# Kernel optimization log

Hardware: AMD Instinct MI355X
Metric: run time of the kernel (lower is better)

## Reference

```python
import jax, jax.numpy as jnp
import numpy as np

B, N, L, H, D = 1, 2048, 256, 24, 128
DX, DY = H * D, 1536          # dim_x = 3072, dim_y = 1536
LV = 200                      # valid text tokens
TOTAL = N + LV                # packed token count
EPS = 1e-6


def rms_norm(t):
    return t * jax.lax.rsqrt(jnp.mean(jnp.square(t), axis=-1, keepdims=True) + EPS)


def setup_inputs() -> dict:
    key = jax.random.key(0)
    ks = jax.random.split(key, 16)
    s = 0.02
    theta = jax.random.uniform(ks[4], (N, H, D // 2), jnp.float32, 0.0, 2.0 * np.pi)
    return {
        "x": jax.random.normal(ks[0], (B, N, DX), jnp.float32),
        "y": jax.random.normal(ks[1], (B, L, DY), jnp.float32),
        "scale_x": jax.random.normal(ks[2], (B, DX), jnp.float32) * 0.1,
        "scale_y": jax.random.normal(ks[3], (B, DY), jnp.float32) * 0.1,
        "rope_cos": jnp.cos(theta),
        "rope_sin": jnp.sin(theta),
        "W_qkv_x": jax.random.normal(ks[5], (3 * DX, DX), jnp.float32) * s,
        "b_qkv_x": jax.random.normal(ks[6], (3 * DX,), jnp.float32) * s,
        "W_qkv_y": jax.random.normal(ks[7], (3 * DX, DY), jnp.float32) * s,
        "b_qkv_y": jax.random.normal(ks[8], (3 * DX,), jnp.float32) * s,
        "q_norm_x": jnp.ones((D,), jnp.float32),
        "k_norm_x": jnp.ones((D,), jnp.float32),
        "q_norm_y": jnp.ones((D,), jnp.float32),
        "k_norm_y": jnp.ones((D,), jnp.float32),
        "W_proj_x": jax.random.normal(ks[9], (DX, DX), jnp.float32) * s,
        "b_proj_x": jax.random.normal(ks[10], (DX,), jnp.float32) * s,
        "W_proj_y": jax.random.normal(ks[11], (DY, DX), jnp.float32) * s,
        "b_proj_y": jax.random.normal(ks[12], (DY,), jnp.float32) * s,
        "valid_token_indices": jnp.arange(TOTAL, dtype=jnp.int64)
        if jax.config.jax_enable_x64 else jnp.arange(TOTAL, dtype=jnp.int32),
    }


def _rope(t, cos, sin):
    # t: (B, N, H, D); cos/sin: (N, H, D/2); real interleaved RoPE
    te, to = t[..., 0::2], t[..., 1::2]
    return jnp.stack([te * cos - to * sin, te * sin + to * cos], axis=-1).reshape(t.shape)


def reference(x, y, scale_x, scale_y, rope_cos, rope_sin,
              W_qkv_x, b_qkv_x, W_qkv_y, b_qkv_y,
              q_norm_x, k_norm_x, q_norm_y, k_norm_y,
              W_proj_x, b_proj_x, W_proj_y, b_proj_y,
              valid_token_indices):
    # modulated RMSNorm + fused qkv projections
    xm = rms_norm(x) * (1.0 + scale_x[:, None, :])                 # (B,N,DX)
    qkv_x = (xm @ W_qkv_x.T + b_qkv_x).reshape(B, N, 3, H, D)
    q_x, k_x, v_x = qkv_x[:, :, 0], qkv_x[:, :, 1], qkv_x[:, :, 2]

    ym = rms_norm(y) * (1.0 + scale_y[:, None, :])                 # (B,L,DY)
    qkv_y = (ym @ W_qkv_y.T + b_qkv_y).reshape(B, L, 3, H, D)
    q_y, k_y, v_y = qkv_y[:, :, 0], qkv_y[:, :, 1], qkv_y[:, :, 2]

    # QK-norm (per-head RMSNorm with learnable weight) + RoPE on visual stream
    q_x = _rope(rms_norm(q_x) * q_norm_x, rope_cos, rope_sin)
    k_x = _rope(rms_norm(k_x) * k_norm_x, rope_cos, rope_sin)
    q_y = rms_norm(q_y) * q_norm_y
    k_y = rms_norm(k_y) * k_norm_y

    # unify_streams: concat streams, gather valid tokens -> packed (TOTAL,H,D)
    q = jnp.concatenate([q_x, q_y], axis=1).reshape(B * (N + L), H, D)[valid_token_indices]
    k = jnp.concatenate([k_x, k_y], axis=1).reshape(B * (N + L), H, D)[valid_token_indices]
    v = jnp.concatenate([v_x, v_y], axis=1).reshape(B * (N + L), H, D)[valid_token_indices]

    # flash varlen attention, B=1 -> single full non-causal segment
    scale = 1.0 / np.sqrt(D)
    scores = jnp.einsum("qhd,khd->hqk", q, k) * scale              # (H,T,T)
    attn = jax.nn.softmax(scores, axis=-1)
    out = jnp.einsum("hqk,khd->qhd", attn, v).reshape(TOTAL, H * D)

    # pad_and_split_xy: scatter packed outputs back to (B, N+L, DX)
    full = jnp.zeros((B * (N + L), H * D), out.dtype).at[valid_token_indices].set(out)
    full = full.reshape(B, N + L, H * D)
    x_out = full[:, :N] @ W_proj_x.T + b_proj_x                    # (B,N,DX)
    y_out = full[:, N:] @ W_proj_y.T + b_proj_y                    # (B,L,DY)
    return x_out, y_out
```

## Files before the change

### kernel.cpp

```cpp
#include <hip/hip_runtime.h>
#include <math.h>

#define NX 2048
#define LY 256
#define NH 24
#define DH 128
#define DXC 3072
#define DYC 1536
#define NLTOK 2304
#define NTOT 2248
#define RMS_EPS 1e-6f

typedef __bf16 bf16x8 __attribute__((ext_vector_type(8)));
typedef float f32x4 __attribute__((ext_vector_type(4)));

static __device__ __forceinline__ unsigned short f2bf(float f) {
    union { float f; unsigned int u; } x; x.f = f;
    unsigned int r = (x.u + 0x7fffu + ((x.u >> 16) & 1u)) >> 16;
    return (unsigned short)r;
}
static __device__ __forceinline__ float bf2f(unsigned short u) {
    union { unsigned int u; float f; } x; x.u = ((unsigned int)u) << 16;
    return x.f;
}
static __device__ __forceinline__ unsigned int pack2(float lo, float hi) {
    return (unsigned int)f2bf(lo) | ((unsigned int)f2bf(hi) << 16);
}
static __device__ __forceinline__ void split4(float4 f, uint2& h, uint2& l) {
    unsigned int ux = __float_as_uint(f.x), uy = __float_as_uint(f.y);
    unsigned int uz = __float_as_uint(f.z), uw = __float_as_uint(f.w);
    h.x = (ux >> 16) | (uy & 0xffff0000u);
    h.y = (uz >> 16) | (uw & 0xffff0000u);
    float lx = f.x - __uint_as_float(ux & 0xffff0000u);
    float ly = f.y - __uint_as_float(uy & 0xffff0000u);
    float lz = f.z - __uint_as_float(uz & 0xffff0000u);
    float lw = f.w - __uint_as_float(uw & 0xffff0000u);
    l.x = pack2(lx, ly);
    l.y = pack2(lz, lw);
}

__global__ __launch_bounds__(256) void rmsnorm_scale_split_kernel(
    const float* __restrict__ in, const float* __restrict__ scale,
    unsigned short* __restrict__ out_hi, unsigned short* __restrict__ out_lo,
    int cols)
{
    const int row = blockIdx.x;
    const int tid = threadIdx.x;
    const float* rp = in + (size_t)row * cols;
    const int nv = cols >> 2;
    float4 vals[3];
    float ss = 0.f;
    int cnt = 0;
    for (int c4 = tid; c4 < nv; c4 += 256) {
        float4 v = ((const float4*)rp)[c4];
        vals[cnt++] = v;
        ss += v.x * v.x + v.y * v.y + v.z * v.z + v.w * v.w;
    }
#pragma unroll
    for (int m = 1; m < 64; m <<= 1) ss += __shfl_xor(ss, m, 64);
    __shared__ float red[4];
    if ((tid & 63) == 0) red[tid >> 6] = ss;
    __syncthreads();
    const float tot = red[0] + red[1] + red[2] + red[3];
    const float r = rsqrtf(tot / (float)cols + RMS_EPS);
    unsigned short* oh = out_hi + (size_t)row * cols;
    unsigned short* ol = out_lo + (size_t)row * cols;
    cnt = 0;
    for (int c4 = tid; c4 < nv; c4 += 256) {
        float4 v = vals[cnt++];
        float4 s = ((const float4*)scale)[c4];
        float4 o;
        o.x = v.x * r * (1.f + s.x);
        o.y = v.y * r * (1.f + s.y);
        o.z = v.z * r * (1.f + s.z);
        o.w = v.w * r * (1.f + s.w);
        uint2 h, l;
        split4(o, h, l);
        ((uint2*)oh)[c4] = h;
        ((uint2*)ol)[c4] = l;
    }
}

__global__ __launch_bounds__(256) void gemm_split_kernel(
    const unsigned short* __restrict__ Ahg, const unsigned short* __restrict__ Alg,
    const float* __restrict__ Bg, const float* __restrict__ bias,
    float* __restrict__ C,
    unsigned short* __restrict__ qp, unsigned short* __restrict__ kp,
    unsigned short* __restrict__ vp,
    int Nc, int K, int mode, int row_off)
{
    __shared__ unsigned short Ah[128 * 40];
    __shared__ unsigned short Al[128 * 40];
    __shared__ unsigned short Bh[128 * 40];
    __shared__ unsigned short Bl[128 * 40];

    const int tid = threadIdx.x;
    const int n0 = blockIdx.x * 128;
    const int m0 = blockIdx.y * 128;
    const int wave = tid >> 6, lane = tid & 63;
    const int quad = lane >> 4, ln = lane & 15;
    const int wm = wave >> 1, wn = wave & 1;
    const int sr = tid >> 1;
    const int sk = (tid & 1) * 16;

    const unsigned short* Abh = Ahg + (size_t)(m0 + sr) * K + sk;
    const unsigned short* Abl = Alg + (size_t)(m0 + sr) * K + sk;
    const float* Bb = Bg + (size_t)(n0 + sr) * K + sk;

    f32x4 acc[4][4];
#pragma unroll
    for (int i = 0; i < 4; ++i)
#pragma unroll
        for (int j = 0; j < 4; ++j) acc[i][j] = (f32x4){0.f, 0.f, 0.f, 0.f};

    uint4 pah0 = *(const uint4*)Abh;
    uint4 pah1 = *(const uint4*)(Abh + 8);
    uint4 pal0 = *(const uint4*)Abl;
    uint4 pal1 = *(const uint4*)(Abl + 8);
    uint4 pbh0, pbh1, pbl0, pbl1;
    {
        float4 b0 = ((const float4*)Bb)[0];
        float4 b1 = ((const float4*)Bb)[1];
        float4 b2 = ((const float4*)Bb)[2];
        float4 b3 = ((const float4*)Bb)[3];
        uint2 h0, l0, h1, l1, h2, l2, h3, l3;
        split4(b0, h0, l0); split4(b1, h1, l1);
        split4(b2, h2, l2); split4(b3, h3, l3);
        pbh0 = make_uint4(h0.x, h0.y, h1.x, h1.y);
        pbh1 = make_uint4(h2.x, h2.y, h3.x, h3.y);
        pbl0 = make_uint4(l0.x, l0.y, l1.x, l1.y);
        pbl1 = make_uint4(l2.x, l2.y, l3.x, l3.y);
    }

    for (int k0 = 0; k0 < K; k0 += 32) {
        __syncthreads();
        *(uint4*)&Ah[sr * 40 + sk]     = pah0;
        *(uint4*)&Ah[sr * 40 + sk + 8] = pah1;
        *(uint4*)&Al[sr * 40 + sk]     = pal0;
        *(uint4*)&Al[sr * 40 + sk + 8] = pal1;
        *(uint4*)&Bh[sr * 40 + sk]     = pbh0;
        *(uint4*)&Bh[sr * 40 + sk + 8] = pbh1;
        *(uint4*)&Bl[sr * 40 + sk]     = pbl0;
        *(uint4*)&Bl[sr * 40 + sk + 8] = pbl1;
        __syncthreads();

        if (k0 + 32 < K) {
            const unsigned short* ah2 = Abh + k0 + 32;
            const unsigned short* al2 = Abl + k0 + 32;
            const float* b2p = Bb + k0 + 32;
            pah0 = *(const uint4*)ah2;  pah1 = *(const uint4*)(ah2 + 8);
            pal0 = *(const uint4*)al2;  pal1 = *(const uint4*)(al2 + 8);
            float4 b0 = ((const float4*)b2p)[0];
            float4 b1 = ((const float4*)b2p)[1];
            float4 b2 = ((const float4*)b2p)[2];
            float4 b3 = ((const float4*)b2p)[3];
            uint2 h0, l0, h1, l1, h2, l2, h3, l3;
            split4(b0, h0, l0); split4(b1, h1, l1);
            split4(b2, h2, l2); split4(b3, h3, l3);
            pbh0 = make_uint4(h0.x, h0.y, h1.x, h1.y);
            pbh1 = make_uint4(h2.x, h2.y, h3.x, h3.y);
            pbl0 = make_uint4(l0.x, l0.y, l1.x, l1.y);
            pbl1 = make_uint4(l2.x, l2.y, l3.x, l3.y);
        }

        bf16x8 afh[4], afl[4];
#pragma unroll
        for (int mt = 0; mt < 4; ++mt) {
            const int rr = (wm * 64 + mt * 16 + ln) * 40 + quad * 8;
            afh[mt] = __builtin_bit_cast(bf16x8, *(const uint4*)&Ah[rr]);
            afl[mt] = __builtin_bit_cast(bf16x8, *(const uint4*)&Al[rr]);
        }
#pragma unroll
        for (int nt = 0; nt < 4; ++nt) {
            const int rr = (wn * 64 + nt * 16 + ln) * 40 + quad * 8;
            bf16x8 bfh = __builtin_bit_cast(bf16x8, *(const uint4*)&Bh[rr]);
            bf16x8 bfl = __builtin_bit_cast(bf16x8, *(const uint4*)&Bl[rr]);
#pragma unroll
            for (int mt = 0; mt < 4; ++mt) {
                acc[mt][nt] = __builtin_amdgcn_mfma_f32_16x16x32_bf16(afh[mt], bfh, acc[mt][nt], 0, 0, 0);
                acc[mt][nt] = __builtin_amdgcn_mfma_f32_16x16x32_bf16(afl[mt], bfh, acc[mt][nt], 0, 0, 0);
                acc[mt][nt] = __builtin_amdgcn_mfma_f32_16x16x32_bf16(afh[mt], bfl, acc[mt][nt], 0, 0, 0);
            }
        }
    }

    float bias4[4];
#pragma unroll
    for (int nt = 0; nt < 4; ++nt) bias4[nt] = bias[n0 + wn * 64 + nt * 16 + ln];

    if (mode == 0) {
#pragma unroll
        for (int mt = 0; mt < 4; ++mt) {
            const int rbase = m0 + wm * 64 + mt * 16 + quad * 4;
#pragma unroll
            for (int reg = 0; reg < 4; ++reg) {
                float* cp = C + (size_t)(rbase + reg) * Nc + n0 + wn * 64 + ln;
#pragma unroll
                for (int nt = 0; nt < 4; ++nt)
                    cp[nt * 16] = acc[mt][nt][reg] + bias4[nt];
            }
        }
    } else {
        const int part = n0 / DXC;
        unsigned short* dst = (part == 0) ? qp : (part == 1) ? kp : vp;
        const int cc = (n0 % DXC) + wn * 64 + ln;
#pragma unroll
        for (int mt = 0; mt < 4; ++mt) {
            const int rbase = row_off + m0 + wm * 64 + mt * 16 + quad * 4;
#pragma unroll
            for (int reg = 0; reg < 4; ++reg) {
                unsigned short* cp = dst + (size_t)(rbase + reg) * DXC + cc;
#pragma unroll
                for (int nt = 0; nt < 4; ++nt)
                    cp[nt * 16] = f2bf(acc[mt][nt][reg] + bias4[nt]);
            }
        }
    }
}

__global__ __launch_bounds__(128) void qknorm_rope_kernel(
    unsigned short* __restrict__ qb, unsigned short* __restrict__ kb,
    const float* __restrict__ qnx, const float* __restrict__ knx,
    const float* __restrict__ qny, const float* __restrict__ kny,
    const float* __restrict__ cosp, const float* __restrict__ sinp)
{
    const int bx = blockIdx.x;
    const int which = bx & 1;
    const int h = (bx >> 1) % NH;
    const int t = bx / (2 * NH);
    unsigned short* p = (which ? kb : qb) + (size_t)t * DXC + h * DH;
    const int d = threadIdx.x;
    const float v = bf2f(p[d]);
    float ss = v * v;
#pragma unroll
    for (int m = 1; m < 64; m <<= 1) ss += __shfl_xor(ss, m, 64);
    __shared__ float red[2];
    if ((d & 63) == 0) red[d >> 6] = ss;
    __syncthreads();
    const float tot = red[0] + red[1];
    const float r = rsqrtf(tot * (1.f / 128.f) + RMS_EPS);
    const float* w = (t < NX) ? (which ? knx : qnx) : (which ? kny : qny);
    const float nv = v * r * w[d];
    float outv = nv;
    if (t < NX) {
        const int pidx = d >> 1;
        const float cs = cosp[((size_t)t * NH + h) * 64 + pidx];
        const float sn = sinp[((size_t)t * NH + h) * 64 + pidx];
        const float partner = __shfl_xor(nv, 1, 64);
        outv = ((d & 1) == 0) ? (nv * cs - partner * sn)
                              : (partner * sn + nv * cs);
    }
    p[d] = f2bf(outv);
}

#define BQ 64
#define BKV 64
#define NQT ((NTOT + BQ - 1) / BQ)
#define ATTN_SCALE 0.08838834764831845f

__global__ __launch_bounds__(256, 3) void attn_kernel(
    const unsigned short* __restrict__ qb, const unsigned short* __restrict__ kb,
    const unsigned short* __restrict__ vb,
    unsigned short* __restrict__ out_hi, unsigned short* __restrict__ out_lo,
    const int* __restrict__ idx)
{
    __shared__ unsigned short Ks[64 * 136];
    __shared__ unsigned int   Vt[128 * 36];
    __shared__ unsigned short Ps[4][16 * 72];

    const int h  = blockIdx.x / NQT;
    const int qt = blockIdx.x % NQT;
    const int q0 = qt * BQ;
    const int tid  = threadIdx.x;
    const int wave = tid >> 6;
    const int lane = tid & 63;
    const int quad = lane >> 4;
    const int ln   = lane & 15;
    const int ch   = tid & 15;
    const int rb   = tid >> 4;

    bf16x8 aq[4];
    {
        const int qi = q0 + wave * 16 + ln;
        if (qi < NTOT) {
            const unsigned short* qrow = qb + (size_t)idx[qi] * DXC + h * DH;
#pragma unroll
            for (int c = 0; c < 4; ++c)
                aq[c] = __builtin_bit_cast(bf16x8, *(const uint4*)(qrow + c * 32 + quad * 8));
        } else {
            const uint4 z = make_uint4(0, 0, 0, 0);
#pragma unroll
            for (int c = 0; c < 4; ++c) aq[c] = __builtin_bit_cast(bf16x8, z);
        }
    }

    f32x4 o[8];
#pragma unroll
    for (int dt = 0; dt < 8; ++dt) o[dt] = (f32x4){0.f, 0.f, 0.f, 0.f};
    float m_i[4] = {-1e30f, -1e30f, -1e30f, -1e30f};
    float l_i[4] = {0.f, 0.f, 0.f, 0.f};

    uint4 kreg[4], vra[2], vrb[2];
    const uint4 z4 = make_uint4(0, 0, 0, 0);
    auto prefetchKV = [&](int kv0) {
#pragma unroll
        for (int it = 0; it < 4; ++it) {
            const int ki = kv0 + rb + it * 16;
            kreg[it] = (ki < NTOT)
                ? *(const uint4*)(kb + (size_t)idx[ki] * DXC + h * DH + ch * 8) : z4;
        }
#pragma unroll
        for (int it = 0; it < 2; ++it) {
            const int pr = rb + it * 16;
            const int k0i = kv0 + pr * 2, k1i = k0i + 1;
            vra[it] = (k0i < NTOT)
                ? *(const uint4*)(vb + (size_t)idx[k0i] * DXC + h * DH + ch * 8) : z4;
            vrb[it] = (k1i < NTOT)
                ? *(const uint4*)(vb + (size_t)idx[k1i] * DXC + h * DH + ch * 8) : z4;
        }
    };
    prefetchKV(0);

    for (int kv0 = 0; kv0 < NTOT; kv0 += BKV) {
        __syncthreads();
#pragma unroll
        for (int it = 0; it < 4; ++it)
            *(uint4*)&Ks[(rb + it * 16) * 136 + ch * 8] = kreg[it];
#pragma unroll
        for (int it = 0; it < 2; ++it) {
            const int pr = rb + it * 16;
            const uint4 a = vra[it], b = vrb[it];
            unsigned int w[8];
            w[0] = (a.x & 0xffffu) | (b.x << 16);  w[1] = (a.x >> 16) | (b.x & 0xffff0000u);
            w[2] = (a.y & 0xffffu) | (b.y << 16);  w[3] = (a.y >> 16) | (b.y & 0xffff0000u);
            w[4] = (a.z & 0xffffu) | (b.z << 16);  w[5] = (a.z >> 16) | (b.z & 0xffff0000u);
            w[6] = (a.w & 0xffffu) | (b.w << 16);  w[7] = (a.w >> 16) | (b.w & 0xffff0000u);
#pragma unroll
            for (int s = 0; s < 8; ++s) {
                const int e = (s + ch) & 7;
                Vt[(ch * 8 + e) * 36 + pr] = w[e];
            }
        }
        __syncthreads();

        if (kv0 + BKV < NTOT) prefetchKV(kv0 + BKV);

        f32x4 sc[4];
        __builtin_amdgcn_s_setprio(1);
#pragma unroll
        for (int t = 0; t < 4; ++t) {
            sc[t] = (f32x4){0.f, 0.f, 0.f, 0.f};
#pragma unroll
            for (int c = 0; c < 4; ++c) {
                bf16x8 bk = __builtin_bit_cast(bf16x8,
                    *(const uint4*)&Ks[(t * 16 + ln) * 136 + c * 32 + quad * 8]);
                sc[t] = __builtin_amdgcn_mfma_f32_16x16x32_bf16(aq[c], bk, sc[t], 0, 0, 0);
            }
        }
        __builtin_amdgcn_s_setprio(0);

        float alpha[4];
#pragma unroll
        for (int r = 0; r < 4; ++r) {
            float mt = -1e30f;
#pragma unroll
            for (int t = 0; t < 4; ++t) {
                float sv = sc[t][r] * ATTN_SCALE;
                if (kv0 + t * 16 + ln >= NTOT) sv = -1e30f;
                sc[t][r] = sv;
                mt = fmaxf(mt, sv);
            }
#pragma unroll
            for (int mm = 1; mm < 16; mm <<= 1) mt = fmaxf(mt, __shfl_xor(mt, mm, 64));
            const float mn = fmaxf(m_i[r], mt);
            alpha[r] = __expf(m_i[r] - mn);
            m_i[r] = mn;
            float rs = 0.f;
#pragma unroll
            for (int t = 0; t < 4; ++t) {
                const float pv = __expf(sc[t][r] - mn);
                sc[t][r] = pv;
                rs += pv;
            }
#pragma unroll
            for (int mm = 1; mm < 16; mm <<= 1) rs += __shfl_xor(rs, mm, 64);
            l_i[r] = l_i[r] * alpha[r] + rs;
        }

        unsigned short* psw = Ps[wave];
#pragma unroll
        for (int t = 0; t < 4; ++t)
#pragma unroll
            for (int r = 0; r < 4; ++r)
                psw[(quad * 4 + r) * 72 + t * 16 + ln] = f2bf(sc[t][r]);

#pragma unroll
        for (int dt = 0; dt < 8; ++dt)
#pragma unroll
            for (int r = 0; r < 4; ++r) o[dt][r] *= alpha[r];

        bf16x8 ap0 = __builtin_bit_cast(bf16x8, *(const uint4*)&psw[ln * 72 + quad * 8]);
        bf16x8 ap1 = __builtin_bit_cast(bf16x8, *(const uint4*)&psw[ln * 72 + 32 + quad * 8]);
        __builtin_amdgcn_s_setprio(1);
#pragma unroll
        for (int dt = 0; dt < 8; ++dt) {
            bf16x8 bv0 = __builtin_bit_cast(bf16x8,
                *(const uint4*)&Vt[(dt * 16 + ln) * 36 + quad * 4]);
            o[dt] = __builtin_amdgcn_mfma_f32_16x16x32_bf16(ap0, bv0, o[dt], 0, 0, 0);
            bf16x8 bv1 = __builtin_bit_cast(bf16x8,
                *(const uint4*)&Vt[(dt * 16 + ln) * 36 + 16 + quad * 4]);
            o[dt] = __builtin_amdgcn_mfma_f32_16x16x32_bf16(ap1, bv1, o[dt], 0, 0, 0);
        }
        __builtin_amdgcn_s_setprio(0);
    }

#pragma unroll
    for (int r = 0; r < 4; ++r) {
        const int qrow = q0 + wave * 16 + quad * 4 + r;
        if (qrow >= NTOT) continue;
        const int tok = idx[qrow];
        const float inv = 1.f / l_i[r];
        unsigned short* hp = out_hi + (size_t)tok * DXC + h * DH + ln;
        unsigned short* lp = out_lo + (size_t)tok * DXC + h * DH + ln;
#pragma unroll
        for (int dt = 0; dt < 8; ++dt) {
            const float v = o[dt][r] * inv;
            const unsigned int u = __float_as_uint(v);
            hp[dt * 16] = (unsigned short)(u >> 16);
            lp[dt * 16] = f2bf(v - __uint_as_float(u & 0xffff0000u));
        }
    }
}

extern "C" void kernel_launch(void* const* d_in, const int* in_sizes, int n_in,
                              void* d_out, int out_size, void* d_ws, size_t ws_size,
                              hipStream_t stream)
{
    const float* x        = (const float*)d_in[0];
    const float* y        = (const float*)d_in[1];
    const float* scale_x  = (const float*)d_in[2];
    const float* scale_y  = (const float*)d_in[3];
    const float* rope_cos = (const float*)d_in[4];
    const float* rope_sin = (const float*)d_in[5];
    const float* W_qkv_x  = (const float*)d_in[6];
    const float* b_qkv_x  = (const float*)d_in[7];
    const float* W_qkv_y  = (const float*)d_in[8];
    const float* b_qkv_y  = (const float*)d_in[9];
    const float* q_norm_x = (const float*)d_in[10];
    const float* k_norm_x = (const float*)d_in[11];
    const float* q_norm_y = (const float*)d_in[12];
    const float* k_norm_y = (const float*)d_in[13];
    const float* W_proj_x = (const float*)d_in[14];
    const float* b_proj_x = (const float*)d_in[15];
    const float* W_proj_y = (const float*)d_in[16];
    const float* b_proj_y = (const float*)d_in[17];
    const int*   vidx     = (const int*)d_in[18];
    float* out = (float*)d_out;

    unsigned short* wsu = (unsigned short*)d_ws;
    const size_t SEG = (size_t)NLTOK * DXC;
    unsigned short* q16     = wsu;
    unsigned short* k16     = wsu + SEG;
    unsigned short* v16     = wsu + 2 * SEG;
    unsigned short* attn_hi = wsu + 3 * SEG;
    unsigned short* attn_lo = wsu + 4 * SEG;
    unsigned short* xm_hi   = wsu + 5 * SEG;
    unsigned short* xm_lo   = wsu + 6 * SEG;
    unsigned short* ym_hi   = xm_hi + (size_t)NX * DXC;
    unsigned short* ym_lo   = xm_lo + (size_t)NX * DXC;

    hipMemsetAsync(attn_hi, 0, 2 * SEG * sizeof(unsigned short), stream);

    rmsnorm_scale_split_kernel<<<NX, 256, 0, stream>>>(x, scale_x, xm_hi, xm_lo, DXC);
    rmsnorm_scale_split_kernel<<<LY, 256, 0, stream>>>(y, scale_y, ym_hi, ym_lo, DYC);

    gemm_split_kernel<<<dim3(9216 / 128, NX / 128), 256, 0, stream>>>(
        xm_hi, xm_lo, W_qkv_x, b_qkv_x, nullptr, q16, k16, v16, 0, DXC, 1, 0);
    gemm_split_kernel<<<dim3(9216 / 128, LY / 128), 256, 0, stream>>>(
        ym_hi, ym_lo, W_qkv_y, b_qkv_y, nullptr, q16, k16, v16, 0, DYC, 1, NX);

    qknorm_rope_kernel<<<NLTOK * NH * 2, 128, 0, stream>>>(
        q16, k16, q_norm_x, k_norm_x, q_norm_y, k_norm_y, rope_cos, rope_sin);

    attn_kernel<<<NH * NQT, 256, 0, stream>>>(q16, k16, v16, attn_hi, attn_lo, vidx);

    gemm_split_kernel<<<dim3(DXC / 128, NX / 128), 256, 0, stream>>>(
        attn_hi, attn_lo, W_proj_x, b_proj_x, out, nullptr, nullptr, nullptr,
        DXC, DXC, 0, 0);
    gemm_split_kernel<<<dim3(DYC / 128, LY / 128), 256, 0, stream>>>(
        attn_hi + (size_t)NX * DXC, attn_lo + (size_t)NX * DXC,
        W_proj_y, b_proj_y, out + (size_t)NX * DXC, nullptr, nullptr, nullptr,
        DYC, DXC, 0, 0);
}
```

Measured before the change: 1.560 ms.

## Split attention KV range across two blocks and merge partials in combine kernel

Attention blocks now each process half of the key/value sequence, doubling the grid to improve CU utilization and reduce tail imbalance. Each split writes unnormalized partial outputs plus running max and sum to a workspace, and a new combine kernel merges them with log-sum-exp weights and scatters to token positions. This adds extra global traffic for the partials, an extra kernel launch, and a memset into reused workspace.

```diff
diff --git a/kernel.cpp b/kernel.cpp
--- a/kernel.cpp
+++ b/kernel.cpp
@@ -9,6 +9,8 @@
 #define DYC 1536
 #define NLTOK 2304
 #define NTOT 2248
+#define KVSPLIT 1124
+#define OPS 130
 #define RMS_EPS 1e-6f
 
 typedef __bf16 bf16x8 __attribute__((ext_vector_type(8)));
@@ -261,7 +263,7 @@
 __global__ __launch_bounds__(256, 3) void attn_kernel(
     const unsigned short* __restrict__ qb, const unsigned short* __restrict__ kb,
     const unsigned short* __restrict__ vb,
-    unsigned short* __restrict__ out_hi, unsigned short* __restrict__ out_lo,
+    unsigned short* __restrict__ ophi, unsigned short* __restrict__ oplo,
     const int* __restrict__ idx)
 {
     __shared__ unsigned short Ks[64 * 136];
@@ -270,6 +272,9 @@
 
     const int h  = blockIdx.x / NQT;
     const int qt = blockIdx.x % NQT;
+    const int s  = blockIdx.y;
+    const int kv_beg = s * KVSPLIT;
+    const int kv_end = (s == 0) ? KVSPLIT : NTOT;
     const int q0 = qt * BQ;
     const int tid  = threadIdx.x;
     const int wave = tid >> 6;
@@ -306,22 +311,22 @@
 #pragma unroll
         for (int it = 0; it < 4; ++it) {
             const int ki = kv0 + rb + it * 16;
-            kreg[it] = (ki < NTOT)
+            kreg[it] = (ki < kv_end)
                 ? *(const uint4*)(kb + (size_t)idx[ki] * DXC + h * DH + ch * 8) : z4;
         }
 #pragma unroll
         for (int it = 0; it < 2; ++it) {
             const int pr = rb + it * 16;
             const int k0i = kv0 + pr * 2, k1i = k0i + 1;
-            vra[it] = (k0i < NTOT)
+            vra[it] = (k0i < kv_end)
                 ? *(const uint4*)(vb + (size_t)idx[k0i] * DXC + h * DH + ch * 8) : z4;
-            vrb[it] = (k1i < NTOT)
+            vrb[it] = (k1i < kv_end)
                 ? *(const uint4*)(vb + (size_t)idx[k1i] * DXC + h * DH + ch * 8) : z4;
         }
     };
-    prefetchKV(0);
-
-    for (int kv0 = 0; kv0 < NTOT; kv0 += BKV) {
+    prefetchKV(kv_beg);
+
+    for (int kv0 = kv_beg; kv0 < kv_end; kv0 += BKV) {
         __syncthreads();
 #pragma unroll
         for (int it = 0; it < 4; ++it)
@@ -336,14 +341,14 @@
             w[4] = (a.z & 0xffffu) | (b.z << 16);  w[5] = (a.z >> 16) | (b.z & 0xffff0000u);
             w[6] = (a.w & 0xffffu) | (b.w << 16);  w[7] = (a.w >> 16) | (b.w & 0xffff0000u);
 #pragma unroll
-            for (int s = 0; s < 8; ++s) {
-                const int e = (s + ch) & 7;
+            for (int ss2 = 0; ss2 < 8; ++ss2) {
+                const int e = (ss2 + ch) & 7;
                 Vt[(ch * 8 + e) * 36 + pr] = w[e];
             }
         }
         __syncthreads();
 
-        if (kv0 + BKV < NTOT) prefetchKV(kv0 + BKV);
+        if (kv0 + BKV < kv_end) prefetchKV(kv0 + BKV);
 
         f32x4 sc[4];
         __builtin_amdgcn_s_setprio(1);
@@ -366,7 +371,7 @@
 #pragma unroll
             for (int t = 0; t < 4; ++t) {
                 float sv = sc[t][r] * ATTN_SCALE;
-                if (kv0 + t * 16 + ln >= NTOT) sv = -1e30f;
+                if (kv0 + t * 16 + ln >= kv_end) sv = -1e30f;
                 sc[t][r] = sv;
                 mt = fmaxf(mt, sv);
             }
@@ -414,22 +419,65 @@
         __builtin_amdgcn_s_setprio(0);
     }
 
+    const size_t obase = (size_t)(s * NH + h) * NTOT;
 #pragma unroll
     for (int r = 0; r < 4; ++r) {
         const int qrow = q0 + wave * 16 + quad * 4 + r;
         if (qrow >= NTOT) continue;
-        const int tok = idx[qrow];
-        const float inv = 1.f / l_i[r];
-        unsigned short* hp = out_hi + (size_t)tok * DXC + h * DH + ln;
-        unsigned short* lp = out_lo + (size_t)tok * DXC + h * DH + ln;
+        const size_t row = obase + qrow;
+        unsigned short* hp = ophi + row * OPS + ln;
+        unsigned short* lp = oplo + row * OPS + ln;
 #pragma unroll
         for (int dt = 0; dt < 8; ++dt) {
-            const float v = o[dt][r] * inv;
+            const float v = o[dt][r];
             const unsigned int u = __float_as_uint(v);
             hp[dt * 16] = (unsigned short)(u >> 16);
             lp[dt * 16] = f2bf(v - __uint_as_float(u & 0xffff0000u));
         }
-    }
+        if (ln == 0) {
+            *(float*)(ophi + row * OPS + DH) = m_i[r];
+            *(float*)(oplo + row * OPS + DH) = l_i[r];
+        }
+    }
+}
+
+__global__ __launch_bounds__(256) void attn_combine_kernel(
+    const unsigned short* __restrict__ ophi, const unsigned short* __restrict__ oplo,
+    unsigned short* __restrict__ out_hi, unsigned short* __restrict__ out_lo,
+    const int* __restrict__ idx)
+{
+    const int wave = threadIdx.x >> 6, lane = threadIdx.x & 63;
+    const int qrow = blockIdx.x * 4 + wave;
+    const int h = blockIdx.y;
+    const size_t r0 = (size_t)h * NTOT + qrow;
+    const size_t r1 = (size_t)(NH + h) * NTOT + qrow;
+    const float m0 = *(const float*)(ophi + r0 * OPS + DH);
+    const float l0 = *(const float*)(oplo + r0 * OPS + DH);
+    const float m1 = *(const float*)(ophi + r1 * OPS + DH);
+    const float l1 = *(const float*)(oplo + r1 * OPS + DH);
+    const float m  = fmaxf(m0, m1);
+    const float w0 = __expf(m0 - m), w1 = __expf(m1 - m);
+    const float inv = 1.f / (l0 * w0 + l1 * w1);
+
+    const ushort2 a0 = *(const ushort2*)(ophi + r0 * OPS + 2 * lane);
+    const ushort2 b0 = *(const ushort2*)(oplo + r0 * OPS + 2 * lane);
+    const ushort2 a1 = *(const ushort2*)(ophi + r1 * OPS + 2 * lane);
+    const ushort2 b1 = *(const ushort2*)(oplo + r1 * OPS + 2 * lane);
+
+    float vx = ((bf2f(a0.x) + bf2f(b0.x)) * w0 + (bf2f(a1.x) + bf2f(b1.x)) * w1) * inv;
+    float vy = ((bf2f(a0.y) + bf2f(b0.y)) * w0 + (bf2f(a1.y) + bf2f(b1.y)) * w1) * inv;
+
+    ushort2 oh, ol;
+    const unsigned int ux = __float_as_uint(vx);
+    oh.x = (unsigned short)(ux >> 16);
+    ol.x = f2bf(vx - __uint_as_float(ux & 0xffff0000u));
+    const unsigned int uy = __float_as_uint(vy);
+    oh.y = (unsigned short)(uy >> 16);
+    ol.y = f2bf(vy - __uint_as_float(uy & 0xffff0000u));
+
+    const size_t doff = (size_t)idx[qrow] * DXC + h * DH + 2 * lane;
+    *(ushort2*)(out_hi + doff) = oh;
+    *(ushort2*)(out_lo + doff) = ol;
 }
 
 extern "C" void kernel_launch(void* const* d_in, const int* in_sizes, int n_in,
@@ -462,14 +510,14 @@
     unsigned short* q16     = wsu;
     unsigned short* k16     = wsu + SEG;
     unsigned short* v16     = wsu + 2 * SEG;
-    unsigned short* attn_hi = wsu + 3 * SEG;
-    unsigned short* attn_lo = wsu + 4 * SEG;
     unsigned short* xm_hi   = wsu + 5 * SEG;
     unsigned short* xm_lo   = wsu + 6 * SEG;
     unsigned short* ym_hi   = xm_hi + (size_t)NX * DXC;
     unsigned short* ym_lo   = xm_lo + (size_t)NX * DXC;
-
-    hipMemsetAsync(attn_hi, 0, 2 * SEG * sizeof(unsigned short), stream);
+    unsigned short* opart_hi = wsu + 3 * SEG;
+    unsigned short* opart_lo = wsu + 5 * SEG;
+    unsigned short* fin_hi = q16;
+    unsigned short* fin_lo = k16;
 
     rmsnorm_scale_split_kernel<<<NX, 256, 0, stream>>>(x, scale_x, xm_hi, xm_lo, DXC);
     rmsnorm_scale_split_kernel<<<LY, 256, 0, stream>>>(y, scale_y, ym_hi, ym_lo, DYC);
@@ -482,13 +530,18 @@
     qknorm_rope_kernel<<<NLTOK * NH * 2, 128, 0, stream>>>(
         q16, k16, q_norm_x, k_norm_x, q_norm_y, k_norm_y, rope_cos, rope_sin);
 
-    attn_kernel<<<NH * NQT, 256, 0, stream>>>(q16, k16, v16, attn_hi, attn_lo, vidx);
+    attn_kernel<<<dim3(NH * NQT, 2), 256, 0, stream>>>(
+        q16, k16, v16, opart_hi, opart_lo, vidx);
+
+    hipMemsetAsync(fin_hi, 0, 2 * SEG * sizeof(unsigned short), stream);
+    attn_combine_kernel<<<dim3(NTOT / 4, NH), 256, 0, stream>>>(
+        opart_hi, opart_lo, fin_hi, fin_lo, vidx);
 
     gemm_split_kernel<<<dim3(DXC / 128, NX / 128), 256, 0, stream>>>(
-        attn_hi, attn_lo, W_proj_x, b_proj_x, out, nullptr, nullptr, nullptr,
+        fin_hi, fin_lo, W_proj_x, b_proj_x, out, nullptr, nullptr, nullptr,
         DXC, DXC, 0, 0);
     gemm_split_kernel<<<dim3(DYC / 128, LY / 128), 256, 0, stream>>>(
-        attn_hi + (size_t)NX * DXC, attn_lo + (size_t)NX * DXC,
+        fin_hi + (size_t)NX * DXC, fin_lo + (size_t)NX * DXC,
         W_proj_y, b_proj_y, out + (size_t)NX * DXC, nullptr, nullptr, nullptr,
         DYC, DXC, 0, 0);
 }
```

Result: faster. 1.480 ms (-5.2%).
